# Optimization experiments

Measured on AMD Instinct MI355X. Metric: run time of the kernel, lower is better.

## Reference

```python
import math
import jax, jax.numpy as jnp
import numpy as np

B, S, D = 8, 1024, 1024
H, DK = 16, 64
NUM_BUCKETS, MAX_DIST = 32, 128


def _relative_position_bucket(relative_position, num_buckets=NUM_BUCKETS, max_distance=MAX_DIST):
    # bidirectional (encoder, is_decoder=False)
    num_buckets //= 2  # 16
    rb = (relative_position > 0).astype(jnp.int32) * num_buckets
    rp = jnp.abs(relative_position)
    max_exact = num_buckets // 2  # 8
    is_small = rp < max_exact
    rp_safe = jnp.maximum(rp, 1)  # avoid log(0); masked out by is_small anyway
    large = max_exact + (
        jnp.log(rp_safe.astype(jnp.float32) / max_exact)
        / math.log(max_distance / max_exact)
        * (num_buckets - max_exact)
    ).astype(jnp.int32)
    large = jnp.minimum(large, num_buckets - 1)
    return rb + jnp.where(is_small, rp, large)


def compute_bias(rel_bias, q_len, k_len):
    ctx = jnp.arange(q_len, dtype=jnp.int32)[:, None]
    mem = jnp.arange(k_len, dtype=jnp.int32)[None, :]
    buckets = _relative_position_bucket(mem - ctx)  # [q_len, k_len]
    vals = rel_bias[buckets]  # [q_len, k_len, H]
    return jnp.transpose(vals, (2, 0, 1))[None]  # [1, H, q_len, k_len]


def setup_inputs() -> dict:
    key = jax.random.key(0)
    ks = jax.random.split(key, 6)
    sd = 1.0 / math.sqrt(D)
    return {
        "hidden_states": jax.random.normal(ks[0], (B, S, D), jnp.float32),
        "wq": jax.random.normal(ks[1], (D, H * DK), jnp.float32) * sd,
        "wk": jax.random.normal(ks[2], (D, H * DK), jnp.float32) * sd,
        "wv": jax.random.normal(ks[3], (D, H * DK), jnp.float32) * sd,
        "wo": jax.random.normal(ks[4], (H * DK, D), jnp.float32) * sd,
        "rel_bias": jax.random.normal(ks[5], (NUM_BUCKETS, H), jnp.float32),
    }


def reference(hidden_states, wq, wk, wv, wo, rel_bias):
    b, s, _ = hidden_states.shape

    def shape_heads(x):  # [b, s, H*DK] -> [b, H, s, DK]
        return jnp.transpose(x.reshape(b, s, H, DK), (0, 2, 1, 3))

    q = shape_heads(hidden_states @ wq)
    k = shape_heads(hidden_states @ wk)
    v = shape_heads(hidden_states @ wv)

    # T5 attention: NO 1/sqrt(dk) scaling
    scores = jnp.einsum("bhqd,bhkd->bhqk", q, k)
    bias = compute_bias(rel_bias, s, s)  # [1, H, s, s]
    attn = jax.nn.softmax(scores + bias, axis=-1)

    ctx = jnp.einsum("bhqk,bhkd->bhqd", attn, v)  # [b, H, s, DK]
    ctx = jnp.transpose(ctx, (0, 2, 1, 3)).reshape(b, s, H * DK)
    return ctx @ wo  # [b, s, D]
```

## Files before the change

kernel.cpp:

```cpp
#include <hip/hip_runtime.h>
#include <stdint.h>

typedef __attribute__((ext_vector_type(8))) short bf16x8;
typedef __attribute__((ext_vector_type(4))) float f32x4;
typedef __attribute__((ext_vector_type(16))) float f32x16;
typedef __attribute__((ext_vector_type(8))) unsigned short ushort8;
typedef __attribute__((ext_vector_type(4))) unsigned short ushort4v;

#define MFMA16(a, b, c) __builtin_amdgcn_mfma_f32_16x16x32_bf16((a), (b), (c), 0, 0, 0)
#define MFMA32(a, b, c) __builtin_amdgcn_mfma_f32_32x32x16_bf16((a), (b), (c), 0, 0, 0)

#define SLEN 1024
#define NHEAD 16
#define HDIM 64
#define DMODEL 1024
#define NROWS 8192
#define LOG2E 1.44269504088896340736f

__device__ __forceinline__ unsigned short f2bf(float f) {
  unsigned int u = __float_as_uint(f);
  u += 0x7FFFu + ((u >> 16) & 1u);
  return (unsigned short)(u >> 16);
}

__device__ __forceinline__ float fast_exp2(float x) {
#if __has_builtin(__builtin_amdgcn_exp2f)
  return __builtin_amdgcn_exp2f(x);
#else
  float r; asm("v_exp_f32 %0, %1" : "=v"(r) : "v"(x)); return r;
#endif
}

__device__ __forceinline__ unsigned int cvt_pk_bf16(float lo, float hi) {
  unsigned int r;
  asm("v_cvt_pk_bf16_f32 %0, %1, %2" : "=v"(r) : "v"(lo), "v"(hi));
  return r;
}

__device__ __forceinline__ void gload_lds16(const void* g, void* l) {
  __builtin_amdgcn_global_load_lds(
      (const __attribute__((address_space(1))) void*)g,
      (__attribute__((address_space(3))) void*)l, 16, 0, 0);
}

__global__ __launch_bounds__(256) void k_convert_x(const float* __restrict__ x,
                                                   unsigned short* __restrict__ xb, int n) {
  int i = blockIdx.x * 256 + threadIdx.x;
  int idx = i * 8;
  if (idx >= n) return;
  float4 a = *(const float4*)(x + idx);
  float4 b = *(const float4*)(x + idx + 4);
  ushort8 o;
  o[0] = f2bf(a.x); o[1] = f2bf(a.y); o[2] = f2bf(a.z); o[3] = f2bf(a.w);
  o[4] = f2bf(b.x); o[5] = f2bf(b.y); o[6] = f2bf(b.z); o[7] = f2bf(b.w);
  *(ushort8*)(xb + idx) = o;
}

__global__ __launch_bounds__(256) void k_transpose_w(
    const float* __restrict__ w0, const float* __restrict__ w1,
    const float* __restrict__ w2, const float* __restrict__ w3,
    unsigned short* __restrict__ o0, unsigned short* __restrict__ o1,
    unsigned short* __restrict__ o2, unsigned short* __restrict__ o3) {
  int z = blockIdx.z;
  const float* w = (z == 0) ? w0 : (z == 1) ? w1 : (z == 2) ? w2 : w3;
  unsigned short* o = (z == 0) ? o0 : (z == 1) ? o1 : (z == 2) ? o2 : o3;
  __shared__ unsigned short tile[32][33];
  int bx = blockIdx.x & 31, by = blockIdx.x >> 5;
  int tid = threadIdx.x;
#pragma unroll
  for (int p = 0; p < 4; ++p) {
    int idx = tid + p * 256;
    int r = idx >> 5, c = idx & 31;
    tile[r][c] = f2bf(w[(size_t)(by * 32 + r) * DMODEL + bx * 32 + c]);
  }
  __syncthreads();
#pragma unroll
  for (int p = 0; p < 4; ++p) {
    int idx = tid + p * 256;
    int r = idx >> 5, c = idx & 31;
    o[(size_t)(bx * 32 + r) * DMODEL + by * 32 + c] = tile[c][r];
  }
}

__global__ __launch_bounds__(256) void k_bias_table(const float* __restrict__ rel_bias,
                                                    float* __restrict__ bt) {
  int i = blockIdx.x * 256 + threadIdx.x;
  if (i >= NHEAD * 2047) return;
  int h = i / 2047, rdx = i % 2047;
  int rel = rdx - 1023;
  int rb = (rel > 0) ? 16 : 0;
  int rp = (rel < 0) ? -rel : rel;
  int bucket;
  if (rp < 8) {
    bucket = rb + rp;
  } else {
    int large;
    if (rp >= 91) {
      large = 15;
    } else {
      int nb = 31 - __clz(rp);
      long long sq = (long long)rp * rp;
      int f2 = 2 * nb + ((sq >= (1LL << (2 * nb + 1))) ? 1 : 0);
      large = 8 + (f2 - 6);
      if (large > 15) large = 15;
    }
    bucket = rb + large;
  }
  bt[h * 2048 + rdx] = rel_bias[bucket * 16 + h] * LOG2E;
}

__device__ __forceinline__ void gemm_tile_lds(const unsigned short* __restrict__ A,
                                              const unsigned short* __restrict__ Bt,
                                              int K, int tm, int tn,
                                              unsigned short* As, unsigned short* Bs,
                                              f32x4 acc[4][4]) {
  const int tid = threadIdx.x;
  const int lane = tid & 63;
  const int w = tid >> 6;
  const int wr = w >> 1, wc = w & 1;
  const int g = lane >> 4, t = lane & 15;
  const int NKT = K >> 5;

  const int c0 = 2 * w, c1 = 2 * w + 1;
  const int r0 = c0 * 16 + (lane >> 2), r1 = c1 * 16 + (lane >> 2);
  const int kc = (lane & 3) * 8;
  const unsigned short* Ag0 = A + (size_t)(tm + r0) * K + kc;
  const unsigned short* Ag1 = A + (size_t)(tm + r1) * K + kc;
  const unsigned short* Bg0 = Bt + (size_t)(tn + r0) * K + kc;
  const unsigned short* Bg1 = Bt + (size_t)(tn + r1) * K + kc;

  f32x4 z = {0.f, 0.f, 0.f, 0.f};
#pragma unroll
  for (int mi = 0; mi < 4; ++mi)
#pragma unroll
    for (int ni = 0; ni < 4; ++ni) acc[mi][ni] = z;

  gload_lds16(Ag0, As + c0 * 512);
  gload_lds16(Ag1, As + c1 * 512);
  gload_lds16(Bg0, Bs + c0 * 512);
  gload_lds16(Bg1, Bs + c1 * 512);
  __syncthreads();

#pragma unroll 1
  for (int kt = 0; kt < NKT; ++kt) {
    const int cur = (kt & 1) * 4096;
    if (kt + 1 < NKT) {
      const int nxt = cur ^ 4096;
      const int ko = (kt + 1) * 32;
      gload_lds16(Ag0 + ko, As + nxt + c0 * 512);
      gload_lds16(Ag1 + ko, As + nxt + c1 * 512);
      gload_lds16(Bg0 + ko, Bs + nxt + c0 * 512);
      gload_lds16(Bg1 + ko, Bs + nxt + c1 * 512);
    }
    bf16x8 af[4], bfr[4];
#pragma unroll
    for (int mi = 0; mi < 4; ++mi)
      af[mi] = *(const bf16x8*)&As[cur + (wr * 64 + mi * 16 + t) * 32 + g * 8];
#pragma unroll
    for (int ni = 0; ni < 4; ++ni)
      bfr[ni] = *(const bf16x8*)&Bs[cur + (wc * 64 + ni * 16 + t) * 32 + g * 8];
#pragma unroll
    for (int mi = 0; mi < 4; ++mi)
#pragma unroll
      for (int ni = 0; ni < 4; ++ni)
        acc[mi][ni] = MFMA16(af[mi], bfr[ni], acc[mi][ni]);
    __syncthreads();
  }
}

__global__ __launch_bounds__(256) void k_gemm_qkv(
    const unsigned short* __restrict__ Xb,
    const unsigned short* __restrict__ Wqt, const unsigned short* __restrict__ Wkt,
    const unsigned short* __restrict__ Wvt,
    unsigned short* __restrict__ Qb, unsigned short* __restrict__ Kb,
    unsigned short* __restrict__ Vt) {
  __shared__ alignas(16) unsigned short As[2 * 128 * 32];
  __shared__ alignas(16) unsigned short Bs[2 * 128 * 32];
  int z = blockIdx.z;
  const unsigned short* Bt = (z == 0) ? Wqt : (z == 1) ? Wkt : Wvt;
  const int wid = (blockIdx.x & 7) * 64 + (blockIdx.x >> 3);
  int tm = (wid >> 3) * 128, tn = (wid & 7) * 128;
  f32x4 acc[4][4];
  gemm_tile_lds(Xb, Bt, DMODEL, tm, tn, As, Bs, acc);

  const int lane = threadIdx.x & 63, w = threadIdx.x >> 6;
  const int wr = w >> 1, wc = w & 1, g = lane >> 4, t = lane & 15;
  if (z < 2) {
    unsigned short* O = (z == 0) ? Qb : Kb;
#pragma unroll
    for (int mi = 0; mi < 4; ++mi)
#pragma unroll
      for (int ni = 0; ni < 4; ++ni)
#pragma unroll
        for (int r = 0; r < 4; ++r) {
          int m = tm + wr * 64 + mi * 16 + g * 4 + r;
          int n = tn + wc * 64 + ni * 16 + t;
          int b = m >> 10, s = m & 1023, h = n >> 6, d = n & 63;
          O[((size_t)((b * 16 + h) * 1024 + s)) * 64 + d] = f2bf(acc[mi][ni][r]);
        }
  } else {
#pragma unroll
    for (int mi = 0; mi < 4; ++mi)
#pragma unroll
      for (int ni = 0; ni < 4; ++ni) {
        int m0 = tm + wr * 64 + mi * 16 + g * 4;
        int n = tn + wc * 64 + ni * 16 + t;
        int b = m0 >> 10, s0 = m0 & 1023, h = n >> 6, d = n & 63;
        ushort4v pk;
#pragma unroll
        for (int r = 0; r < 4; ++r) pk[r] = f2bf(acc[mi][ni][r]);
        *(ushort4v*)&Vt[((size_t)((b * 16 + h) * 64 + d) * 1024) + s0] = pk;
      }
  }
}

__global__ __launch_bounds__(512) void k_attn(
    const unsigned short* __restrict__ Qb, const unsigned short* __restrict__ Kb,
    const unsigned short* __restrict__ Vt, const float* __restrict__ bt,
    unsigned short* __restrict__ ctx) {
  __shared__ alignas(16) unsigned short Ks[2][64 * 64];
  __shared__ alignas(16) unsigned short Vs[2][64 * 64];
  __shared__ alignas(16) float Lb[376];
  __shared__ float sred[8][32];

  const int wid = ((blockIdx.x & 7) << 6) | (blockIdx.x >> 3);
  const int bh = wid >> 2, qb = wid & 3;
  const int h = bh & 15, b = bh >> 4;
  const int tid = threadIdx.x;
  const int lane = tid & 63, w = tid >> 6;
  const int ql = lane & 31, hi = lane >> 5;
  const int q0 = qb * 256 + w * 32;
  const int q = q0 + ql;

  for (int i = tid; i < 376; i += 512) Lb[i] = bt[(size_t)h * 2048 + 837 + i];

  const unsigned short* Qp = Qb + (size_t)bh * SLEN * 64;
  const unsigned short* Kp = Kb + (size_t)bh * SLEN * 64;
  const unsigned short* Vp = Vt + (size_t)bh * 64 * SLEN;

  bf16x8 bq[4];
#pragma unroll
  for (int c = 0; c < 4; ++c)
    bq[c] = *(const bf16x8*)(Qp + (size_t)q * 64 + c * 16 + hi * 8);

  const f32x16 z16 = {0.f,0.f,0.f,0.f,0.f,0.f,0.f,0.f,0.f,0.f,0.f,0.f,0.f,0.f,0.f,0.f};
  f32x16 o0 = z16, o1 = z16;
  float m = -INFINITY, l = 0.f;

  auto stage = [&](int buf, int kbase) {
    int lb = w * 1024 + lane * 16;
    int row = lb >> 7;
    int lc = ((lb >> 4) & 7) ^ (row & 7);
    gload_lds16(Kp + (size_t)(kbase + row) * 64 + lc * 8, &Ks[buf][w * 512]);
    gload_lds16(Vp + (size_t)row * SLEN + kbase + lc * 8, &Vs[buf][w * 512]);
  };

  stage(0, 0);
  __syncthreads();
  const float cpos = Lb[186 + 91], cneg = Lb[186 - 91];

  int cur = 0;
#pragma unroll 1
  for (int kt = 0; kt < 16; ++kt) {
    const int kbase = kt * 64;
    if (kt != 15) stage(cur ^ 1, kbase + 64);

    const char* Kc = (const char*)Ks[cur];
    const char* Vc = (const char*)Vs[cur];

#pragma unroll
    for (int hh = 0; hh < 2; ++hh) {
      const int kb32 = kbase + hh * 32;

      bf16x8 ak[4];
#pragma unroll
      for (int c = 0; c < 4; ++c) {
        const int ph = ((c << 1) | hi) ^ (ql & 7);
        ak[c] = *(const bf16x8*)(Kc + (hh * 32 + ql) * 128 + ph * 16);
      }

      bf16x8 bv00, bv01, bv10, bv11;
      {
        const int p0 = ((hh << 2) | hi) ^ (ql & 7);
        const int p1 = ((hh << 2) | 2 | hi) ^ (ql & 7);
        bv00 = *(const bf16x8*)(Vc + ql * 128 + p0 * 16);
        bv01 = *(const bf16x8*)(Vc + (32 + ql) * 128 + p0 * 16);
        bv10 = *(const bf16x8*)(Vc + ql * 128 + p1 * 16);
        bv11 = *(const bf16x8*)(Vc + (32 + ql) * 128 + p1 * 16);
      }

      f32x16 s = z16;
      __builtin_amdgcn_s_setprio(1);
#pragma unroll
      for (int c = 0; c < 4; ++c) s = MFMA32(ak[c], bq[c], s);
      __builtin_amdgcn_s_setprio(0);

      const bool farp = (kb32 >= q0 + 122);
      const bool farn = (kb32 + 122 <= q0);
      if (farp || farn) {
        const float c = farp ? cpos : cneg;
#pragma unroll
        for (int r = 0; r < 16; ++r) s[r] = fmaf(s[r], LOG2E, c);
      } else {
        const int base = kb32 - q + 186 + hi * 4;
#pragma unroll
        for (int r = 0; r < 16; ++r)
          s[r] = fmaf(s[r], LOG2E, Lb[base + (r & 3) + 8 * (r >> 2)]);
      }

      float vm = s[0];
#pragma unroll
      for (int r = 1; r < 16; ++r) vm = fmaxf(vm, s[r]);
      vm = fmaxf(vm, __shfl_xor(vm, 32));

      if (__any(vm > m + 8.0f)) {
        const float mn = fmaxf(m, vm);
        const float sc = fast_exp2(m - mn);
        m = mn;
        l *= sc;
        sred[w][ql] = sc;
        __builtin_amdgcn_wave_barrier();
#pragma unroll
        for (int r = 0; r < 16; ++r) {
          const float sr = sred[w][(r & 3) + 8 * (r >> 2) + hi * 4];
          o0[r] *= sr; o1[r] *= sr;
        }
        __builtin_amdgcn_wave_barrier();
      }

      float p[16];
      float ls = 0.f;
#pragma unroll
      for (int r = 0; r < 16; ++r) { p[r] = fast_exp2(s[r] - m); ls += p[r]; }
      l += ls + __shfl_xor(ls, 32);

      unsigned int wv[8], xv[8];
#pragma unroll
      for (int i = 0; i < 8; ++i) wv[i] = cvt_pk_bf16(p[2 * i], p[2 * i + 1]);
#pragma unroll
      for (int i = 0; i < 8; ++i) xv[i] = __shfl_xor(wv[i], 32);
      union { unsigned int u[4]; bf16x8 v; } pa0, pa1;
      pa0.u[0] = hi ? xv[2] : wv[0];
      pa0.u[1] = hi ? xv[3] : wv[1];
      pa0.u[2] = hi ? wv[2] : xv[0];
      pa0.u[3] = hi ? wv[3] : xv[1];
      pa1.u[0] = hi ? xv[6] : wv[4];
      pa1.u[1] = hi ? xv[7] : wv[5];
      pa1.u[2] = hi ? wv[6] : xv[4];
      pa1.u[3] = hi ? wv[7] : xv[5];

      __builtin_amdgcn_s_setprio(1);
      o0 = MFMA32(pa0.v, bv00, o0);
      o0 = MFMA32(pa1.v, bv10, o0);
      o1 = MFMA32(pa0.v, bv01, o1);
      o1 = MFMA32(pa1.v, bv11, o1);
      __builtin_amdgcn_s_setprio(0);
    }

    __syncthreads();
    cur ^= 1;
  }

  const float inv = 1.0f / l;
  sred[w][ql] = inv;
  __builtin_amdgcn_wave_barrier();
#pragma unroll
  for (int r = 0; r < 16; ++r) {
    const float ir = sred[w][(r & 3) + 8 * (r >> 2) + hi * 4];
    const int qq = q0 + (r & 3) + 8 * (r >> 2) + hi * 4;
    const size_t base = ((size_t)(b * 1024 + qq)) * 1024 + h * 64 + ql;
    ctx[base] = f2bf(o0[r] * ir);
    ctx[base + 32] = f2bf(o1[r] * ir);
  }
}

__global__ __launch_bounds__(256) void k_gemm_out(
    const unsigned short* __restrict__ Cb, const unsigned short* __restrict__ Wot,
    float* __restrict__ out) {
  __shared__ alignas(16) unsigned short As[2 * 128 * 32];
  __shared__ alignas(16) unsigned short Bs[2 * 128 * 32];
  const int wid = (blockIdx.x & 7) * 64 + (blockIdx.x >> 3);
  int tm = (wid >> 3) * 128, tn = (wid & 7) * 128;
  f32x4 acc[4][4];
  gemm_tile_lds(Cb, Wot, DMODEL, tm, tn, As, Bs, acc);

  const int lane = threadIdx.x & 63, w = threadIdx.x >> 6;
  const int wr = w >> 1, wc = w & 1, g = lane >> 4, t = lane & 15;
#pragma unroll
  for (int mi = 0; mi < 4; ++mi)
#pragma unroll
    for (int ni = 0; ni < 4; ++ni)
#pragma unroll
      for (int r = 0; r < 4; ++r) {
        int m = tm + wr * 64 + mi * 16 + g * 4 + r;
        int n = tn + wc * 64 + ni * 16 + t;
        out[(size_t)m * DMODEL + n] = acc[mi][ni][r];
      }
}

extern "C" void kernel_launch(void* const* d_in, const int* in_sizes, int n_in,
                              void* d_out, int out_size, void* d_ws, size_t ws_size,
                              hipStream_t stream) {
  const float* hs = (const float*)d_in[0];
  const float* wq = (const float*)d_in[1];
  const float* wk = (const float*)d_in[2];
  const float* wv = (const float*)d_in[3];
  const float* wo = (const float*)d_in[4];
  const float* rb = (const float*)d_in[5];

  char* ws = (char*)d_ws;
  unsigned short* Xb  = (unsigned short*)(ws + 0);
  unsigned short* Wqt = (unsigned short*)(ws + 16777216);
  unsigned short* Wkt = (unsigned short*)(ws + 18874368);
  unsigned short* Wvt = (unsigned short*)(ws + 20971520);
  unsigned short* Wot = (unsigned short*)(ws + 23068672);
  unsigned short* Qb  = (unsigned short*)(ws + 25165824);
  unsigned short* Kb  = (unsigned short*)(ws + 41943040);
  unsigned short* Vt  = (unsigned short*)(ws + 58720256);
  unsigned short* Cb  = (unsigned short*)(ws + 75497472);
  float* bt           = (float*)(ws + 92274688);

  k_convert_x<<<4096, 256, 0, stream>>>(hs, Xb, NROWS * DMODEL);
  k_transpose_w<<<dim3(1024, 1, 4), 256, 0, stream>>>(wq, wk, wv, wo, Wqt, Wkt, Wvt, Wot);
  k_bias_table<<<128, 256, 0, stream>>>(rb, bt);
  k_gemm_qkv<<<dim3(512, 1, 3), 256, 0, stream>>>(Xb, Wqt, Wkt, Wvt, Qb, Kb, Vt);
  k_attn<<<512, 512, 0, stream>>>(Qb, Kb, Vt, bt, Cb);
  k_gemm_out<<<512, 256, 0, stream>>>(Cb, Wot, (float*)d_out);
}
```

Measured before the change: 187.7 us.

## Triple-buffer GEMM LDS staging with two tiles in flight and vmcnt waits

Moves the shared GEMM tile loop from double to triple buffering in LDS. It prefetches two K-tiles ahead and replaces __syncthreads with explicit s_waitcnt vmcnt plus s_barrier, so one tile's global-to-LDS loads can still be in flight while the next is consumed. The aim is to hide global load latency in the QKV and output projections. In exchange, LDS use per block grows by half, which may lower occupancy, and correctness now depends on the hand-written vmcnt counts.

```diff
diff --git a/kernel.cpp b/kernel.cpp
--- a/kernel.cpp
+++ b/kernel.cpp
@@ -129,42 +129,47 @@
   const unsigned short* Bg0 = Bt + (size_t)(tn + r0) * K + kc;
   const unsigned short* Bg1 = Bt + (size_t)(tn + r1) * K + kc;
 
+  auto stageT = [&](int off, int kt2) {
+    const int ko = kt2 * 32;
+    gload_lds16(Ag0 + ko, As + off + c0 * 512);
+    gload_lds16(Ag1 + ko, As + off + c1 * 512);
+    gload_lds16(Bg0 + ko, Bs + off + c0 * 512);
+    gload_lds16(Bg1 + ko, Bs + off + c1 * 512);
+  };
+
   f32x4 z = {0.f, 0.f, 0.f, 0.f};
 #pragma unroll
   for (int mi = 0; mi < 4; ++mi)
 #pragma unroll
     for (int ni = 0; ni < 4; ++ni) acc[mi][ni] = z;
 
-  gload_lds16(Ag0, As + c0 * 512);
-  gload_lds16(Ag1, As + c1 * 512);
-  gload_lds16(Bg0, Bs + c0 * 512);
-  gload_lds16(Bg1, Bs + c1 * 512);
-  __syncthreads();
-
+  stageT(0, 0);
+  stageT(4096, 1);
+  asm volatile("s_waitcnt vmcnt(4)" ::: "memory");
+  __builtin_amdgcn_s_barrier();
+
+  int oc = 0, on = 4096, of = 8192;
 #pragma unroll 1
   for (int kt = 0; kt < NKT; ++kt) {
-    const int cur = (kt & 1) * 4096;
-    if (kt + 1 < NKT) {
-      const int nxt = cur ^ 4096;
-      const int ko = (kt + 1) * 32;
-      gload_lds16(Ag0 + ko, As + nxt + c0 * 512);
-      gload_lds16(Ag1 + ko, As + nxt + c1 * 512);
-      gload_lds16(Bg0 + ko, Bs + nxt + c0 * 512);
-      gload_lds16(Bg1 + ko, Bs + nxt + c1 * 512);
-    }
+    if (kt + 2 < NKT) stageT(of, kt + 2);
+
     bf16x8 af[4], bfr[4];
 #pragma unroll
     for (int mi = 0; mi < 4; ++mi)
-      af[mi] = *(const bf16x8*)&As[cur + (wr * 64 + mi * 16 + t) * 32 + g * 8];
+      af[mi] = *(const bf16x8*)&As[oc + (wr * 64 + mi * 16 + t) * 32 + g * 8];
 #pragma unroll
     for (int ni = 0; ni < 4; ++ni)
-      bfr[ni] = *(const bf16x8*)&Bs[cur + (wc * 64 + ni * 16 + t) * 32 + g * 8];
+      bfr[ni] = *(const bf16x8*)&Bs[oc + (wc * 64 + ni * 16 + t) * 32 + g * 8];
 #pragma unroll
     for (int mi = 0; mi < 4; ++mi)
 #pragma unroll
       for (int ni = 0; ni < 4; ++ni)
         acc[mi][ni] = MFMA16(af[mi], bfr[ni], acc[mi][ni]);
-    __syncthreads();
+
+    if (kt + 2 < NKT) asm volatile("s_waitcnt vmcnt(4)" ::: "memory");
+    else              asm volatile("s_waitcnt vmcnt(0)" ::: "memory");
+    __builtin_amdgcn_s_barrier();
+    const int tmp = oc; oc = on; on = of; of = tmp;
   }
 }
 
@@ -174,8 +179,8 @@
     const unsigned short* __restrict__ Wvt,
     unsigned short* __restrict__ Qb, unsigned short* __restrict__ Kb,
     unsigned short* __restrict__ Vt) {
-  __shared__ alignas(16) unsigned short As[2 * 128 * 32];
-  __shared__ alignas(16) unsigned short Bs[2 * 128 * 32];
+  __shared__ alignas(16) unsigned short As[3 * 128 * 32];
+  __shared__ alignas(16) unsigned short Bs[3 * 128 * 32];
   int z = blockIdx.z;
   const unsigned short* Bt = (z == 0) ? Wqt : (z == 1) ? Wkt : Wvt;
   const int wid = (blockIdx.x & 7) * 64 + (blockIdx.x >> 3);
@@ -377,8 +382,8 @@
 __global__ __launch_bounds__(256) void k_gemm_out(
     const unsigned short* __restrict__ Cb, const unsigned short* __restrict__ Wot,
     float* __restrict__ out) {
-  __shared__ alignas(16) unsigned short As[2 * 128 * 32];
-  __shared__ alignas(16) unsigned short Bs[2 * 128 * 32];
+  __shared__ alignas(16) unsigned short As[3 * 128 * 32];
+  __shared__ alignas(16) unsigned short Bs[3 * 128 * 32];
   const int wid = (blockIdx.x & 7) * 64 + (blockIdx.x >> 3);
   int tm = (wid >> 3) * 128, tn = (wid & 7) * 128;
   f32x4 acc[4][4];
```

After: 191.6 us. 1.02x slower.

## Double GEMM K-tile to 64 with XOR-swizzled LDS layout

Applied to the files above, without the earlier changes.

The shared GEMM tile routine now stages 64-wide K slices instead of 32, which halves the number of barriers and main-loop iterations. It also stores A and B tiles in LDS with an XOR swizzle on 16-byte chunks so that fragment reads avoid bank conflicts. LDS use per block doubles to 64 KB, which may limit occupancy for both the QKV and output projection kernels.

```diff
diff --git a/kernel.cpp b/kernel.cpp
--- a/kernel.cpp
+++ b/kernel.cpp
@@ -119,15 +119,17 @@
   const int w = tid >> 6;
   const int wr = w >> 1, wc = w & 1;
   const int g = lane >> 4, t = lane & 15;
-  const int NKT = K >> 5;
-
-  const int c0 = 2 * w, c1 = 2 * w + 1;
-  const int r0 = c0 * 16 + (lane >> 2), r1 = c1 * 16 + (lane >> 2);
-  const int kc = (lane & 3) * 8;
-  const unsigned short* Ag0 = A + (size_t)(tm + r0) * K + kc;
-  const unsigned short* Ag1 = A + (size_t)(tm + r1) * K + kc;
-  const unsigned short* Bg0 = Bt + (size_t)(tn + r0) * K + kc;
-  const unsigned short* Bg1 = Bt + (size_t)(tn + r1) * K + kc;
+  const int NKT = K >> 6;
+
+  auto stageT = [&](int bufo, int ko) {
+#pragma unroll
+    for (int j = 0; j < 4; ++j) {
+      const int r = w * 32 + j * 8 + (lane >> 3);
+      const int lc = (lane & 7) ^ (r & 7);
+      gload_lds16(A + (size_t)(tm + r) * K + ko + lc * 8, As + bufo + (w * 4 + j) * 512);
+      gload_lds16(Bt + (size_t)(tn + r) * K + ko + lc * 8, Bs + bufo + (w * 4 + j) * 512);
+    }
+  };
 
   f32x4 z = {0.f, 0.f, 0.f, 0.f};
 #pragma unroll
@@ -135,35 +137,39 @@
 #pragma unroll
     for (int ni = 0; ni < 4; ++ni) acc[mi][ni] = z;
 
-  gload_lds16(Ag0, As + c0 * 512);
-  gload_lds16(Ag1, As + c1 * 512);
-  gload_lds16(Bg0, Bs + c0 * 512);
-  gload_lds16(Bg1, Bs + c1 * 512);
+  stageT(0, 0);
   __syncthreads();
 
 #pragma unroll 1
   for (int kt = 0; kt < NKT; ++kt) {
-    const int cur = (kt & 1) * 4096;
-    if (kt + 1 < NKT) {
-      const int nxt = cur ^ 4096;
-      const int ko = (kt + 1) * 32;
-      gload_lds16(Ag0 + ko, As + nxt + c0 * 512);
-      gload_lds16(Ag1 + ko, As + nxt + c1 * 512);
-      gload_lds16(Bg0 + ko, Bs + nxt + c0 * 512);
-      gload_lds16(Bg1 + ko, Bs + nxt + c1 * 512);
-    }
-    bf16x8 af[4], bfr[4];
-#pragma unroll
-    for (int mi = 0; mi < 4; ++mi)
-      af[mi] = *(const bf16x8*)&As[cur + (wr * 64 + mi * 16 + t) * 32 + g * 8];
-#pragma unroll
-    for (int ni = 0; ni < 4; ++ni)
-      bfr[ni] = *(const bf16x8*)&Bs[cur + (wc * 64 + ni * 16 + t) * 32 + g * 8];
-#pragma unroll
-    for (int mi = 0; mi < 4; ++mi)
-#pragma unroll
-      for (int ni = 0; ni < 4; ++ni)
-        acc[mi][ni] = MFMA16(af[mi], bfr[ni], acc[mi][ni]);
+    const int cur = (kt & 1) * 8192;
+    if (kt + 1 < NKT) stageT(cur ^ 8192, (kt + 1) * 64);
+
+    bf16x8 af[2][4], bfr[2][4];
+#pragma unroll
+    for (int kk = 0; kk < 2; ++kk)
+#pragma unroll
+      for (int mi = 0; mi < 4; ++mi) {
+        const int ra = wr * 64 + mi * 16 + t;
+        const int pa = ((kk << 2) | g) ^ (ra & 7);
+        af[kk][mi] = *(const bf16x8*)&As[cur + ra * 64 + pa * 8];
+      }
+#pragma unroll
+    for (int kk = 0; kk < 2; ++kk)
+#pragma unroll
+      for (int ni = 0; ni < 4; ++ni) {
+        const int rb = wc * 64 + ni * 16 + t;
+        const int pb = ((kk << 2) | g) ^ (rb & 7);
+        bfr[kk][ni] = *(const bf16x8*)&Bs[cur + rb * 64 + pb * 8];
+      }
+#pragma unroll
+    for (int kk = 0; kk < 2; ++kk)
+#pragma unroll
+      for (int mi = 0; mi < 4; ++mi)
+#pragma unroll
+        for (int ni = 0; ni < 4; ++ni)
+          acc[mi][ni] = MFMA16(af[kk][mi], bfr[kk][ni], acc[mi][ni]);
+
     __syncthreads();
   }
 }
@@ -174,8 +180,8 @@
     const unsigned short* __restrict__ Wvt,
     unsigned short* __restrict__ Qb, unsigned short* __restrict__ Kb,
     unsigned short* __restrict__ Vt) {
-  __shared__ alignas(16) unsigned short As[2 * 128 * 32];
-  __shared__ alignas(16) unsigned short Bs[2 * 128 * 32];
+  __shared__ alignas(16) unsigned short As[2 * 128 * 64];
+  __shared__ alignas(16) unsigned short Bs[2 * 128 * 64];
   int z = blockIdx.z;
   const unsigned short* Bt = (z == 0) ? Wqt : (z == 1) ? Wkt : Wvt;
   const int wid = (blockIdx.x & 7) * 64 + (blockIdx.x >> 3);
@@ -377,8 +383,8 @@
 __global__ __launch_bounds__(256) void k_gemm_out(
     const unsigned short* __restrict__ Cb, const unsigned short* __restrict__ Wot,
     float* __restrict__ out) {
-  __shared__ alignas(16) unsigned short As[2 * 128 * 32];
-  __shared__ alignas(16) unsigned short Bs[2 * 128 * 32];
+  __shared__ alignas(16) unsigned short As[2 * 128 * 64];
+  __shared__ alignas(16) unsigned short Bs[2 * 128 * 64];
   const int wid = (blockIdx.x & 7) * 64 + (blockIdx.x >> 3);
   int tm = (wid >> 3) * 128, tn = (wid & 7) * 128;
   f32x4 acc[4][4];
```

Measured after the change: 171.4 us. -8.7%, faster.
